# Optimization experiments

Measured on AMD Instinct MI355X. Metric: run time of the kernel, lower is better.

## Reference

```python
import jax, jax.numpy as jnp
import numpy as np

IH, IW = 48, 48           # img_size
C = 256                   # inp == oup
NH, HD = 8, 32            # num_heads, head_dims; inner_dim = 256
HID = 4 * C               # MLP hidden
N = IH * IW               # window size (seq len) = 2304
SCALE = (C // NH) ** -0.5 # (inp_dims // num_heads) ** -0.5
EPS = 1e-5


def _relative_position_index():
    coords = np.stack(np.meshgrid(np.arange(IH), np.arange(IW), indexing='ij'))
    cf = coords.reshape(2, -1)
    rel = (cf[:, :, None] - cf[:, None, :]).transpose(1, 2, 0)
    rel[:, :, 0] += IH - 1
    rel[:, :, 1] += IW - 1
    rel[:, :, 0] *= 2 * IW - 1
    return jnp.asarray(rel.sum(-1).astype(np.int32))  # [N, N]


def setup_inputs() -> dict:
    key = jax.random.key(0)
    ks = jax.random.split(key, 12)
    s = 0.02
    return {
        'x': jax.random.normal(ks[0], (1, IH, IW, C), jnp.float32),
        'gamma1': jnp.ones((C,), jnp.float32),
        'beta1': jnp.zeros((C,), jnp.float32),
        'w_qkv': jax.random.normal(ks[1], (C, 3 * NH * HD), jnp.float32) * s,
        'w_proj': jax.random.normal(ks[2], (NH * HD, C), jnp.float32) * s,
        'b_proj': jnp.zeros((C,), jnp.float32),
        'bias_table': jax.random.normal(ks[3], ((2 * IH - 1) * (2 * IW - 1), NH), jnp.float32) * s,
        'gamma2': jnp.ones((C,), jnp.float32),
        'beta2': jnp.zeros((C,), jnp.float32),
        'w_fc1': jax.random.normal(ks[4], (C, HID), jnp.float32) * s,
        'b_fc1': jnp.zeros((HID,), jnp.float32),
        'w_fc2': jax.random.normal(ks[5], (HID, C), jnp.float32) * s,
        'b_fc2': jnp.zeros((C,), jnp.float32),
        'rel_idx': _relative_position_index(),
    }


def _layernorm(x, g, b):
    mu = jnp.mean(x, axis=-1, keepdims=True)
    var = jnp.mean(jnp.square(x - mu), axis=-1, keepdims=True)
    return (x - mu) * jax.lax.rsqrt(var + EPS) * g + b


def reference(x, gamma1, beta1, w_qkv, w_proj, b_proj, bias_table,
              gamma2, beta2, w_fc1, b_fc1, w_fc2, b_fc2, rel_idx):
    shortcut = x                                   # [1, IH, IW, C]
    t = x.reshape(1, N, C)
    t = _layernorm(t, gamma1, beta1)

    # qkv: [1, N, 3*NH*HD] -> q, k, v each [1, NH, N, HD]
    qkv = (t @ w_qkv).reshape(1, N, 3, NH, HD).transpose(2, 0, 3, 1, 4)
    q, k, v = qkv[0], qkv[1], qkv[2]
    q = q * SCALE

    attn = jnp.einsum('bhnd,bhmd->bhnm', q, k)     # [1, NH, N, N]
    # relative position bias: gather table rows by index -> [NH, N, N]
    bias = bias_table[rel_idx.reshape(-1)].reshape(N, N, NH).transpose(2, 0, 1)
    attn = jax.nn.softmax(attn + bias[None], axis=-1)

    o = jnp.einsum('bhnm,bhmd->bhnd', attn, v)     # [1, NH, N, HD]
    o = o.transpose(0, 2, 1, 3).reshape(1, N, NH * HD)
    o = o @ w_proj + b_proj                        # [1, N, C]

    x = shortcut + o.reshape(1, IH, IW, C)
    shortcut = x

    t = _layernorm(x.reshape(1, N, C), gamma2, beta2)
    t = jax.nn.gelu(t @ w_fc1 + b_fc1, approximate=False) @ w_fc2 + b_fc2
    return shortcut + t.reshape(1, IH, IW, C)
```

## Files before the change

### kernel.cpp

```cpp
#include <hip/hip_runtime.h>
#include <hip/hip_bf16.h>
#include <math.h>

#define IH 48
#define IW 48
#define NN 2304
#define CC 256
#define NH 8
#define HD 32
#define HID 1024
#define NBIAS 9025
#define SCALE 0.17677669529663687f
#define LOG2E 1.4426950408889634f
#define LN_EPS 1e-5f

typedef __attribute__((ext_vector_type(8))) short bf16x8;
typedef __attribute__((ext_vector_type(4))) float f32x4;

__device__ __forceinline__ short f2b(float f) {
    __hip_bfloat16 h = __float2bfloat16(f);
    short s; __builtin_memcpy(&s, &h, 2); return s;
}
__device__ __forceinline__ float b2f(short s) {
    __hip_bfloat16 h; __builtin_memcpy(&h, &s, 2); return __bfloat162float(h);
}
__device__ __forceinline__ float fast_exp2(float x) {
#if __has_builtin(__builtin_amdgcn_exp2f)
    return __builtin_amdgcn_exp2f(x);
#else
    return exp2f(x);
#endif
}

__global__ void prep_kernel(const float* __restrict__ x, const float* __restrict__ g,
                            const float* __restrict__ b, short* __restrict__ t1,
                            const float* __restrict__ bt, short* __restrict__ o_bias)
{
    const int bid = blockIdx.x, tid = threadIdx.x;
    if (bid < NN) {
        __shared__ float red[8];
        float v = x[bid * CC + tid];
        float s = v, s2 = v * v;
        #pragma unroll
        for (int off = 32; off > 0; off >>= 1) {
            s  += __shfl_xor(s, off);
            s2 += __shfl_xor(s2, off);
        }
        const int wid = tid >> 6;
        if ((tid & 63) == 0) { red[wid * 2] = s; red[wid * 2 + 1] = s2; }
        __syncthreads();
        float tot  = red[0] + red[2] + red[4] + red[6];
        float tot2 = red[1] + red[3] + red[5] + red[7];
        float mu   = tot * (1.0f / CC);
        float var  = tot2 * (1.0f / CC) - mu * mu;
        float rstd = rsqrtf(var + LN_EPS);
        t1[bid * CC + tid] = f2b((v - mu) * rstd * g[tid] + b[tid]);
        return;
    }
    const int stride = (gridDim.x - NN) * 256;
    for (int i = (bid - NN) * 256 + tid; i < NBIAS * NH; i += stride) {
        int idx = i >> 3, h = i & 7;
        o_bias[h * NBIAS + idx] = f2b(bt[i] * LOG2E);
    }
}

__global__ void wtrans_kernel(const float* __restrict__ w_qkv, const float* __restrict__ w_proj,
                              const float* __restrict__ w_fc1, const float* __restrict__ w_fc2,
                              short* __restrict__ o_qkv, short* __restrict__ o_proj,
                              short* __restrict__ o_fc1, short* __restrict__ o_fc2)
{
    __shared__ float t[32][33];
    int b = blockIdx.x;
    const float* src; short* dst; int K, Nn, kt, nt;
    if (b < 192)      { src = w_qkv;  dst = o_qkv;  K = 256;  Nn = 768;  kt = b / 24; nt = b % 24; }
    else if (b < 256) { b -= 192; src = w_proj; dst = o_proj; K = 256;  Nn = 256;  kt = b / 8;  nt = b % 8; }
    else if (b < 512) { b -= 256; src = w_fc1;  dst = o_fc1;  K = 256;  Nn = 1024; kt = b / 32; nt = b % 32; }
    else              { b -= 512; src = w_fc2;  dst = o_fc2;  K = 1024; Nn = 256;  kt = b / 8;  nt = b % 8; }
    const int r = threadIdx.x >> 5, c = threadIdx.x & 31;
    const int k0 = kt * 32, n0 = nt * 32;
    #pragma unroll
    for (int i = 0; i < 4; ++i)
        t[r + i * 8][c] = src[(k0 + r + i * 8) * Nn + n0 + c];
    __syncthreads();
    #pragma unroll
    for (int i = 0; i < 4; ++i)
        dst[(n0 + r + i * 8) * K + k0 + c] = f2b(t[c][r + i * 8]);
}

__global__ void ln_kernel(const float* __restrict__ p0, const float* __restrict__ p1,
                          const float* __restrict__ bp, const float* __restrict__ x_in,
                          const float* __restrict__ g, const float* __restrict__ b,
                          short* __restrict__ t2, float* __restrict__ x2)
{
    __shared__ float red[8];
    const int row = blockIdx.x, tid = threadIdx.x;
    const int i = row * CC + tid;
    float v = p0[i] + p1[i] + bp[tid] + x_in[i];
    x2[i] = v;
    float s = v, s2 = v * v;
    #pragma unroll
    for (int off = 32; off > 0; off >>= 1) {
        s  += __shfl_xor(s, off);
        s2 += __shfl_xor(s2, off);
    }
    const int wid = tid >> 6;
    if ((tid & 63) == 0) { red[wid * 2] = s; red[wid * 2 + 1] = s2; }
    __syncthreads();
    float tot  = red[0] + red[2] + red[4] + red[6];
    float tot2 = red[1] + red[3] + red[5] + red[7];
    float mu   = tot * (1.0f / CC);
    float var  = tot2 * (1.0f / CC) - mu * mu;
    float rstd = rsqrtf(var + LN_EPS);
    t2[i] = f2b((v - mu) * rstd * g[tid] + b[tid]);
}

#define GSTRIDE 72
template<int KLEN, int KSTR>
__device__ __forceinline__ void mfma_gemm_core(const short* __restrict__ A,
                                               const short* __restrict__ BT,
                                               int m0, int n0, int kb, f32x4 acc[4],
                                               short* lds)
{
    short* As = lds;
    short* Bs = lds + 64 * GSTRIDE;
    const int tid  = threadIdx.x;
    const int w    = tid >> 6, lane = tid & 63;
    const int quad = lane >> 4, l15 = lane & 15;
    const int sr = tid >> 2;
    const int sc = (tid & 3) * 16;
    #pragma unroll
    for (int c = 0; c < 4; ++c) acc[c] = (f32x4){0.f, 0.f, 0.f, 0.f};

    const short* Ap = &A [(m0 + sr) * KSTR + kb + sc];
    const short* Bp = &BT[(n0 + sr) * KSTR + kb + sc];
    bf16x8 ra0 = *(const bf16x8*)Ap,       ra1 = *(const bf16x8*)(Ap + 8);
    bf16x8 rb0 = *(const bf16x8*)Bp,       rb1 = *(const bf16x8*)(Bp + 8);

    for (int k0 = 0; k0 < KLEN; k0 += 64) {
        __syncthreads();
        *(bf16x8*)&As[sr * GSTRIDE + sc]     = ra0;
        *(bf16x8*)&As[sr * GSTRIDE + sc + 8] = ra1;
        *(bf16x8*)&Bs[sr * GSTRIDE + sc]     = rb0;
        *(bf16x8*)&Bs[sr * GSTRIDE + sc + 8] = rb1;
        if (k0 + 64 < KLEN) {
            ra0 = *(const bf16x8*)(Ap + k0 + 64);
            ra1 = *(const bf16x8*)(Ap + k0 + 72);
            rb0 = *(const bf16x8*)(Bp + k0 + 64);
            rb1 = *(const bf16x8*)(Bp + k0 + 72);
        }
        __syncthreads();
        #pragma unroll
        for (int s = 0; s < 2; ++s) {
            bf16x8 a = *(const bf16x8*)&As[(w * 16 + l15) * GSTRIDE + s * 32 + quad * 8];
            #pragma unroll
            for (int c = 0; c < 4; ++c) {
                bf16x8 b = *(const bf16x8*)&Bs[(c * 16 + l15) * GSTRIDE + s * 32 + quad * 8];
                acc[c] = __builtin_amdgcn_mfma_f32_16x16x32_bf16(a, b, acc[c], 0, 0, 0);
            }
        }
    }
}

__global__ void qkv_kernel(const short* __restrict__ t1, const short* __restrict__ wT,
                           short* __restrict__ qb, short* __restrict__ kb,
                           short* __restrict__ vT)
{
    __shared__ short lds[2 * 64 * GSTRIDE];
    f32x4 acc[4];
    const int m0 = blockIdx.y * 64, n0 = blockIdx.x * 64;
    mfma_gemm_core<256, 256>(t1, wT, m0, n0, 0, acc, lds);
    const int lane = threadIdx.x & 63, w = threadIdx.x >> 6;
    const int quad = lane >> 4, l15 = lane & 15;
    #pragma unroll
    for (int c = 0; c < 4; ++c) {
        int col = n0 + c * 16 + l15;
        int three = col >> 8, rem = col & 255;
        int h = rem >> 5, d = rem & 31;
        #pragma unroll
        for (int r = 0; r < 4; ++r) {
            int row = m0 + w * 16 + quad * 4 + r;
            float v = acc[c][r];
            if (three == 0)      qb[(h * NN + row) * HD + d] = f2b(v * (SCALE * LOG2E));
            else if (three == 1) kb[(h * NN + row) * HD + d] = f2b(v);
            else                 vT[(h * HD + d) * NN + row] = f2b(v);
        }
    }
}

#define PSTRIDE 40
__global__ __launch_bounds__(256) void attn_kernel(
        const short* __restrict__ qb, const short* __restrict__ kb,
        const short* __restrict__ vT, const short* __restrict__ biasT,
        short* __restrict__ o)
{
    __shared__ float Ored[4][16][33];
    __shared__ float lred[4][16];
    __shared__ short sbuf[4][16 * PSTRIDE];
    __shared__ short bwin[48][64];
    const int w = threadIdx.x >> 6, lane = threadIdx.x & 63;
    const int quad = lane >> 4, l15 = lane & 15;
    const int h = blockIdx.x / 144, q0 = (blockIdx.x % 144) * 16;
    const int t0 = w * 576;
    short* sb = &sbuf[w][0];
    const short* bt = &biasT[h * NBIAS];

    const int qi = q0 / IW, qj0 = q0 % IW;

    for (int idx = threadIdx.x; idx < 48 * 63; idx += 256) {
        int kr = idx / 63, cc = idx - kr * 63;
        bwin[kr][cc] = bt[(qi - kr + 47) * 95 + qj0 + cc];
    }

    bf16x8 qf = *(const bf16x8*)&qb[(h * NN + q0 + l15) * HD + quad * 8];

    f32x4 O0 = (f32x4){0.f,0.f,0.f,0.f}, O1 = (f32x4){0.f,0.f,0.f,0.f};
    float lp[4] = {0.f, 0.f, 0.f, 0.f};
    const f32x4 zero = (f32x4){0.f,0.f,0.f,0.f};

    __syncthreads();

    for (int c = 0; c < 18; ++c) {
        const int t = t0 + c * 32;
        bf16x8 k0f = *(const bf16x8*)&kb[(h * NN + t      + l15) * HD + quad * 8];
        bf16x8 k1f = *(const bf16x8*)&kb[(h * NN + t + 16 + l15) * HD + quad * 8];
        f32x4 s0 = __builtin_amdgcn_mfma_f32_16x16x32_bf16(qf, k0f, zero, 0, 0, 0);
        f32x4 s1 = __builtin_amdgcn_mfma_f32_16x16x32_bf16(qf, k1f, zero, 0, 0, 0);
        bf16x8 v0 = *(const bf16x8*)&vT[(h * HD + l15)      * NN + t + quad * 8];
        bf16x8 v1 = *(const bf16x8*)&vT[(h * HD + 16 + l15) * NN + t + quad * 8];

        const int ki0 = t / IW,        kj0_ = t - ki0 * IW;
        const int ki1 = (t + 16) / IW, kj1_ = (t + 16) - ki1 * IW;
        const int cA = quad * 4 + 47 - kj0_ - l15;
        const int cB = quad * 4 + 47 - kj1_ - l15;

        #pragma unroll
        for (int r = 0; r < 4; ++r) {
            float p0 = fast_exp2(s0[r] + b2f(bwin[ki0][cA + r]));
            float p1 = fast_exp2(s1[r] + b2f(bwin[ki1][cB + r]));
            lp[r] += p0 + p1;
            sb[(quad * 4 + r) * PSTRIDE + l15]      = f2b(p0);
            sb[(quad * 4 + r) * PSTRIDE + 16 + l15] = f2b(p1);
        }
        asm volatile("s_waitcnt lgkmcnt(0)" ::: "memory");
        bf16x8 pa = *(const bf16x8*)&sb[l15 * PSTRIDE + quad * 8];
        O0 = __builtin_amdgcn_mfma_f32_16x16x32_bf16(pa, v0, O0, 0, 0, 0);
        O1 = __builtin_amdgcn_mfma_f32_16x16x32_bf16(pa, v1, O1, 0, 0, 0);
    }

    #pragma unroll
    for (int r = 0; r < 4; ++r) {
        float l = lp[r];
        l += __shfl_xor(l, 1); l += __shfl_xor(l, 2);
        l += __shfl_xor(l, 4); l += __shfl_xor(l, 8);
        if (l15 == 0) lred[w][quad * 4 + r] = l;
        Ored[w][quad * 4 + r][l15]      = O0[r];
        Ored[w][quad * 4 + r][16 + l15] = O1[r];
    }
    __syncthreads();
    {
        const int col = threadIdx.x & 31;
        for (int rr = threadIdx.x >> 5; rr < 16; rr += 8) {
            float s = 0.f, l = 0.f;
            #pragma unroll
            for (int pw = 0; pw < 4; ++pw) { s += Ored[pw][rr][col]; l += lred[pw][rr]; }
            o[(q0 + rr) * CC + h * HD + col] = f2b(s / l);
        }
    }
}

__global__ void proj_kernel(const short* __restrict__ o, const short* __restrict__ wT,
                            float* __restrict__ Ppj)
{
    __shared__ short lds[2 * 64 * GSTRIDE];
    f32x4 acc[4];
    const int m0 = blockIdx.y * 64, n0 = blockIdx.x * 64, z = blockIdx.z;
    mfma_gemm_core<128, 256>(o, wT, m0, n0, z * 128, acc, lds);
    const int lane = threadIdx.x & 63, w = threadIdx.x >> 6;
    const int quad = lane >> 4, l15 = lane & 15;
    float* out = Ppj + z * (NN * CC);
    #pragma unroll
    for (int c = 0; c < 4; ++c) {
        int col = n0 + c * 16 + l15;
        #pragma unroll
        for (int r = 0; r < 4; ++r) {
            int row = m0 + w * 16 + quad * 4 + r;
            out[row * CC + col] = acc[c][r];
        }
    }
}

__global__ void fc1_kernel(const short* __restrict__ t2, const short* __restrict__ wT,
                           const float* __restrict__ bias, short* __restrict__ h1)
{
    __shared__ short lds[2 * 64 * GSTRIDE];
    f32x4 acc[4];
    const int m0 = blockIdx.y * 64, n0 = blockIdx.x * 64;
    mfma_gemm_core<256, 256>(t2, wT, m0, n0, 0, acc, lds);
    const int lane = threadIdx.x & 63, w = threadIdx.x >> 6;
    const int quad = lane >> 4, l15 = lane & 15;
    #pragma unroll
    for (int c = 0; c < 4; ++c) {
        int col = n0 + c * 16 + l15;
        #pragma unroll
        for (int r = 0; r < 4; ++r) {
            int row = m0 + w * 16 + quad * 4 + r;
            float v = acc[c][r] + bias[col];
            float ge = 0.5f * v * (1.0f + erff(v * 0.7071067811865476f));
            h1[row * HID + col] = f2b(ge);
        }
    }
}

__global__ void fc2_kernel(const short* __restrict__ h1, const short* __restrict__ wT,
                           float* __restrict__ Pfc)
{
    __shared__ short lds[2 * 64 * GSTRIDE];
    f32x4 acc[4];
    const int m0 = blockIdx.y * 64, n0 = blockIdx.x * 64, z = blockIdx.z;
    mfma_gemm_core<512, 1024>(h1, wT, m0, n0, z * 512, acc, lds);
    const int lane = threadIdx.x & 63, w = threadIdx.x >> 6;
    const int quad = lane >> 4, l15 = lane & 15;
    float* out = Pfc + z * (NN * CC);
    #pragma unroll
    for (int c = 0; c < 4; ++c) {
        int col = n0 + c * 16 + l15;
        #pragma unroll
        for (int r = 0; r < 4; ++r) {
            int row = m0 + w * 16 + quad * 4 + r;
            out[row * CC + col] = acc[c][r];
        }
    }
}

__global__ void fc2_red(const float* __restrict__ Pfc, const float* __restrict__ bias,
                        const float* __restrict__ x2, float* __restrict__ out)
{
    const int i = blockIdx.x * CC + threadIdx.x;
    const int NC = NN * CC;
    out[i] = Pfc[i] + Pfc[NC + i] + bias[threadIdx.x] + x2[i];
}

extern "C" void kernel_launch(void* const* d_in, const int* in_sizes, int n_in,
                              void* d_out, int out_size, void* d_ws, size_t ws_size,
                              hipStream_t stream)
{
    const float* x          = (const float*)d_in[0];
    const float* gamma1     = (const float*)d_in[1];
    const float* beta1      = (const float*)d_in[2];
    const float* w_qkv      = (const float*)d_in[3];
    const float* w_proj     = (const float*)d_in[4];
    const float* b_proj     = (const float*)d_in[5];
    const float* bias_table = (const float*)d_in[6];
    const float* gamma2     = (const float*)d_in[7];
    const float* beta2      = (const float*)d_in[8];
    const float* w_fc1      = (const float*)d_in[9];
    const float* b_fc1      = (const float*)d_in[10];
    const float* w_fc2      = (const float*)d_in[11];
    const float* b_fc2      = (const float*)d_in[12];

    short* S = (short*)d_ws;
    const int NC = NN * CC;
    short* t1     = S;
    short* qb     = t1  + NC;
    short* kb     = qb  + NC;
    short* vT     = kb  + NC;
    short* obuf   = vT  + NC;
    short* t2     = obuf+ NC;
    short* h1     = t2  + NC;
    short* wTqkv  = h1  + NN * HID;
    short* wTproj = wTqkv  + 768 * 256;
    short* wTfc1  = wTproj + 256 * 256;
    short* wTfc2  = wTfc1  + 1024 * 256;
    short* biasT  = wTfc2  + 256 * 1024;
    float* x2     = (float*)(biasT + NH * NBIAS + 8);
    float* Ppj    = (float*)t1;
    float* Pfc    = (float*)t1;

    prep_kernel<<<NN + 64, 256, 0, stream>>>(x, gamma1, beta1, t1,
                                             bias_table, biasT);
    wtrans_kernel<<<768, 256, 0, stream>>>(w_qkv, w_proj, w_fc1, w_fc2,
                                           wTqkv, wTproj, wTfc1, wTfc2);
    qkv_kernel<<<dim3(12, 36), 256, 0, stream>>>(t1, wTqkv, qb, kb, vT);
    attn_kernel<<<1152, 256, 0, stream>>>(qb, kb, vT, biasT, obuf);
    proj_kernel<<<dim3(4, 36, 2), 256, 0, stream>>>(obuf, wTproj, Ppj);
    ln_kernel<<<NN, 256, 0, stream>>>(Ppj, Ppj + NC, b_proj, x,
                                      gamma2, beta2, t2, x2);
    fc1_kernel<<<dim3(16, 36), 256, 0, stream>>>(t2, wTfc1, b_fc1, h1);
    fc2_kernel<<<dim3(4, 36, 2), 256, 0, stream>>>(h1, wTfc2, Pfc);
    fc2_red<<<NN, 256, 0, stream>>>(Pfc, b_fc2, x2, (float*)d_out);
}
```

Measured before the change: 169.1 us.

## Drop split-K partials in proj/fc2, fuse bias+residual epilogues, merge weight transpose into prep

Merges the weight-transpose kernel into the prep kernel, saving one launch. The proj and fc2 GEMMs stop using a two-way split-K with fp32 partial buffers. They now run full K with 32-row tiles and 128-thread blocks, adding bias and residual in the epilogue. This removes the separate fc2 reduction kernel and the partial-sum traffic, and ln_kernel now only normalizes x2. The cost is longer per-block K loops with fewer waves per block, which reduces latency hiding in the GEMMs.

```diff
diff --git a/kernel.cpp b/kernel.cpp
--- a/kernel.cpp
+++ b/kernel.cpp
@@ -34,11 +34,16 @@
 
 __global__ void prep_kernel(const float* __restrict__ x, const float* __restrict__ g,
                             const float* __restrict__ b, short* __restrict__ t1,
-                            const float* __restrict__ bt, short* __restrict__ o_bias)
-{
+                            const float* __restrict__ bt, short* __restrict__ o_bias,
+                            const float* __restrict__ w_qkv, const float* __restrict__ w_proj,
+                            const float* __restrict__ w_fc1, const float* __restrict__ w_fc2,
+                            short* __restrict__ o_qkv, short* __restrict__ o_proj,
+                            short* __restrict__ o_fc1, short* __restrict__ o_fc2)
+{
+    __shared__ float tsh[32][33];
+    __shared__ float red[8];
     const int bid = blockIdx.x, tid = threadIdx.x;
     if (bid < NN) {
-        __shared__ float red[8];
         float v = x[bid * CC + tid];
         float s = v, s2 = v * v;
         #pragma unroll
@@ -57,46 +62,39 @@
         t1[bid * CC + tid] = f2b((v - mu) * rstd * g[tid] + b[tid]);
         return;
     }
-    const int stride = (gridDim.x - NN) * 256;
-    for (int i = (bid - NN) * 256 + tid; i < NBIAS * NH; i += stride) {
+    if (bid < NN + 768) {
+        int bb = bid - NN;
+        const float* src; short* dst; int K, Nn, kt, nt;
+        if (bb < 192)      { src = w_qkv;  dst = o_qkv;  K = 256;  Nn = 768;  kt = bb / 24; nt = bb % 24; }
+        else if (bb < 256) { bb -= 192; src = w_proj; dst = o_proj; K = 256;  Nn = 256;  kt = bb / 8;  nt = bb % 8; }
+        else if (bb < 512) { bb -= 256; src = w_fc1;  dst = o_fc1;  K = 256;  Nn = 1024; kt = bb / 32; nt = bb % 32; }
+        else               { bb -= 512; src = w_fc2;  dst = o_fc2;  K = 1024; Nn = 256;  kt = bb / 8;  nt = bb % 8; }
+        const int r = tid >> 5, c = tid & 31;
+        const int k0 = kt * 32, n0 = nt * 32;
+        #pragma unroll
+        for (int i = 0; i < 4; ++i)
+            tsh[r + i * 8][c] = src[(k0 + r + i * 8) * Nn + n0 + c];
+        __syncthreads();
+        #pragma unroll
+        for (int i = 0; i < 4; ++i)
+            dst[(n0 + r + i * 8) * K + k0 + c] = f2b(tsh[c][r + i * 8]);
+        return;
+    }
+    const int stride = (gridDim.x - NN - 768) * 256;
+    for (int i = (bid - NN - 768) * 256 + tid; i < NBIAS * NH; i += stride) {
         int idx = i >> 3, h = i & 7;
         o_bias[h * NBIAS + idx] = f2b(bt[i] * LOG2E);
     }
 }
 
-__global__ void wtrans_kernel(const float* __restrict__ w_qkv, const float* __restrict__ w_proj,
-                              const float* __restrict__ w_fc1, const float* __restrict__ w_fc2,
-                              short* __restrict__ o_qkv, short* __restrict__ o_proj,
-                              short* __restrict__ o_fc1, short* __restrict__ o_fc2)
-{
-    __shared__ float t[32][33];
-    int b = blockIdx.x;
-    const float* src; short* dst; int K, Nn, kt, nt;
-    if (b < 192)      { src = w_qkv;  dst = o_qkv;  K = 256;  Nn = 768;  kt = b / 24; nt = b % 24; }
-    else if (b < 256) { b -= 192; src = w_proj; dst = o_proj; K = 256;  Nn = 256;  kt = b / 8;  nt = b % 8; }
-    else if (b < 512) { b -= 256; src = w_fc1;  dst = o_fc1;  K = 256;  Nn = 1024; kt = b / 32; nt = b % 32; }
-    else              { b -= 512; src = w_fc2;  dst = o_fc2;  K = 1024; Nn = 256;  kt = b / 8;  nt = b % 8; }
-    const int r = threadIdx.x >> 5, c = threadIdx.x & 31;
-    const int k0 = kt * 32, n0 = nt * 32;
-    #pragma unroll
-    for (int i = 0; i < 4; ++i)
-        t[r + i * 8][c] = src[(k0 + r + i * 8) * Nn + n0 + c];
-    __syncthreads();
-    #pragma unroll
-    for (int i = 0; i < 4; ++i)
-        dst[(n0 + r + i * 8) * K + k0 + c] = f2b(t[c][r + i * 8]);
-}
-
-__global__ void ln_kernel(const float* __restrict__ p0, const float* __restrict__ p1,
-                          const float* __restrict__ bp, const float* __restrict__ x_in,
-                          const float* __restrict__ g, const float* __restrict__ b,
-                          short* __restrict__ t2, float* __restrict__ x2)
+__global__ void ln_kernel(const float* __restrict__ x,
+                          const float* __restrict__ g,
+                          const float* __restrict__ b,
+                          short* __restrict__ out)
 {
     __shared__ float red[8];
     const int row = blockIdx.x, tid = threadIdx.x;
-    const int i = row * CC + tid;
-    float v = p0[i] + p1[i] + bp[tid] + x_in[i];
-    x2[i] = v;
+    float v = x[row * CC + tid];
     float s = v, s2 = v * v;
     #pragma unroll
     for (int off = 32; off > 0; off >>= 1) {
@@ -111,18 +109,18 @@
     float mu   = tot * (1.0f / CC);
     float var  = tot2 * (1.0f / CC) - mu * mu;
     float rstd = rsqrtf(var + LN_EPS);
-    t2[i] = f2b((v - mu) * rstd * g[tid] + b[tid]);
+    out[row * CC + tid] = f2b((v - mu) * rstd * g[tid] + b[tid]);
 }
 
 #define GSTRIDE 72
-template<int KLEN, int KSTR>
+template<int KLEN, int KSTR, int TM>
 __device__ __forceinline__ void mfma_gemm_core(const short* __restrict__ A,
                                                const short* __restrict__ BT,
                                                int m0, int n0, int kb, f32x4 acc[4],
                                                short* lds)
 {
     short* As = lds;
-    short* Bs = lds + 64 * GSTRIDE;
+    short* Bs = lds + TM * GSTRIDE;
     const int tid  = threadIdx.x;
     const int w    = tid >> 6, lane = tid & 63;
     const int quad = lane >> 4, l15 = lane & 15;
@@ -135,6 +133,12 @@
     const short* Bp = &BT[(n0 + sr) * KSTR + kb + sc];
     bf16x8 ra0 = *(const bf16x8*)Ap,       ra1 = *(const bf16x8*)(Ap + 8);
     bf16x8 rb0 = *(const bf16x8*)Bp,       rb1 = *(const bf16x8*)(Bp + 8);
+    bf16x8 rc0, rc1;
+    const short* Bp2 = Bp;
+    if constexpr (TM == 32) {
+        Bp2 = &BT[(n0 + sr + 32) * KSTR + kb + sc];
+        rc0 = *(const bf16x8*)Bp2;  rc1 = *(const bf16x8*)(Bp2 + 8);
+    }
 
     for (int k0 = 0; k0 < KLEN; k0 += 64) {
         __syncthreads();
@@ -142,11 +146,19 @@
         *(bf16x8*)&As[sr * GSTRIDE + sc + 8] = ra1;
         *(bf16x8*)&Bs[sr * GSTRIDE + sc]     = rb0;
         *(bf16x8*)&Bs[sr * GSTRIDE + sc + 8] = rb1;
+        if constexpr (TM == 32) {
+            *(bf16x8*)&Bs[(sr + 32) * GSTRIDE + sc]     = rc0;
+            *(bf16x8*)&Bs[(sr + 32) * GSTRIDE + sc + 8] = rc1;
+        }
         if (k0 + 64 < KLEN) {
             ra0 = *(const bf16x8*)(Ap + k0 + 64);
             ra1 = *(const bf16x8*)(Ap + k0 + 72);
             rb0 = *(const bf16x8*)(Bp + k0 + 64);
             rb1 = *(const bf16x8*)(Bp + k0 + 72);
+            if constexpr (TM == 32) {
+                rc0 = *(const bf16x8*)(Bp2 + k0 + 64);
+                rc1 = *(const bf16x8*)(Bp2 + k0 + 72);
+            }
         }
         __syncthreads();
         #pragma unroll
@@ -168,7 +180,7 @@
     __shared__ short lds[2 * 64 * GSTRIDE];
     f32x4 acc[4];
     const int m0 = blockIdx.y * 64, n0 = blockIdx.x * 64;
-    mfma_gemm_core<256, 256>(t1, wT, m0, n0, 0, acc, lds);
+    mfma_gemm_core<256, 256, 64>(t1, wT, m0, n0, 0, acc, lds);
     const int lane = threadIdx.x & 63, w = threadIdx.x >> 6;
     const int quad = lane >> 4, l15 = lane & 15;
     #pragma unroll
@@ -269,22 +281,22 @@
 }
 
 __global__ void proj_kernel(const short* __restrict__ o, const short* __restrict__ wT,
-                            float* __restrict__ Ppj)
-{
-    __shared__ short lds[2 * 64 * GSTRIDE];
+                            const float* __restrict__ bias, const float* __restrict__ x_in,
+                            float* __restrict__ x2)
+{
+    __shared__ short lds[(32 + 64) * GSTRIDE];
     f32x4 acc[4];
-    const int m0 = blockIdx.y * 64, n0 = blockIdx.x * 64, z = blockIdx.z;
-    mfma_gemm_core<128, 256>(o, wT, m0, n0, z * 128, acc, lds);
+    const int m0 = blockIdx.y * 32, n0 = blockIdx.x * 64;
+    mfma_gemm_core<256, 256, 32>(o, wT, m0, n0, 0, acc, lds);
     const int lane = threadIdx.x & 63, w = threadIdx.x >> 6;
     const int quad = lane >> 4, l15 = lane & 15;
-    float* out = Ppj + z * (NN * CC);
     #pragma unroll
     for (int c = 0; c < 4; ++c) {
         int col = n0 + c * 16 + l15;
         #pragma unroll
         for (int r = 0; r < 4; ++r) {
             int row = m0 + w * 16 + quad * 4 + r;
-            out[row * CC + col] = acc[c][r];
+            x2[row * CC + col] = acc[c][r] + bias[col] + x_in[row * CC + col];
         }
     }
 }
@@ -295,7 +307,7 @@
     __shared__ short lds[2 * 64 * GSTRIDE];
     f32x4 acc[4];
     const int m0 = blockIdx.y * 64, n0 = blockIdx.x * 64;
-    mfma_gemm_core<256, 256>(t2, wT, m0, n0, 0, acc, lds);
+    mfma_gemm_core<256, 256, 64>(t2, wT, m0, n0, 0, acc, lds);
     const int lane = threadIdx.x & 63, w = threadIdx.x >> 6;
     const int quad = lane >> 4, l15 = lane & 15;
     #pragma unroll
@@ -312,32 +324,24 @@
 }
 
 __global__ void fc2_kernel(const short* __restrict__ h1, const short* __restrict__ wT,
-                           float* __restrict__ Pfc)
-{
-    __shared__ short lds[2 * 64 * GSTRIDE];
+                           const float* __restrict__ bias, const float* __restrict__ x2,
+                           float* __restrict__ out)
+{
+    __shared__ short lds[(32 + 64) * GSTRIDE];
     f32x4 acc[4];
-    const int m0 = blockIdx.y * 64, n0 = blockIdx.x * 64, z = blockIdx.z;
-    mfma_gemm_core<512, 1024>(h1, wT, m0, n0, z * 512, acc, lds);
+    const int m0 = blockIdx.y * 32, n0 = blockIdx.x * 64;
+    mfma_gemm_core<1024, 1024, 32>(h1, wT, m0, n0, 0, acc, lds);
     const int lane = threadIdx.x & 63, w = threadIdx.x >> 6;
     const int quad = lane >> 4, l15 = lane & 15;
-    float* out = Pfc + z * (NN * CC);
     #pragma unroll
     for (int c = 0; c < 4; ++c) {
         int col = n0 + c * 16 + l15;
         #pragma unroll
         for (int r = 0; r < 4; ++r) {
             int row = m0 + w * 16 + quad * 4 + r;
-            out[row * CC + col] = acc[c][r];
-        }
-    }
-}
-
-__global__ void fc2_red(const float* __restrict__ Pfc, const float* __restrict__ bias,
-                        const float* __restrict__ x2, float* __restrict__ out)
-{
-    const int i = blockIdx.x * CC + threadIdx.x;
-    const int NC = NN * CC;
-    out[i] = Pfc[i] + Pfc[NC + i] + bias[threadIdx.x] + x2[i];
+            out[row * CC + col] = acc[c][r] + bias[col] + x2[row * CC + col];
+        }
+    }
 }
 
 extern "C" void kernel_launch(void* const* d_in, const int* in_sizes, int n_in,
@@ -373,19 +377,16 @@
     short* wTfc2  = wTfc1  + 1024 * 256;
     short* biasT  = wTfc2  + 256 * 1024;
     float* x2     = (float*)(biasT + NH * NBIAS + 8);
-    float* Ppj    = (float*)t1;
-    float* Pfc    = (float*)t1;
-
-    prep_kernel<<<NN + 64, 256, 0, stream>>>(x, gamma1, beta1, t1,
-                                             bias_table, biasT);
-    wtrans_kernel<<<768, 256, 0, stream>>>(w_qkv, w_proj, w_fc1, w_fc2,
-                                           wTqkv, wTproj, wTfc1, wTfc2);
+
+    prep_kernel<<<NN + 768 + 64, 256, 0, stream>>>(x, gamma1, beta1, t1,
+                                                   bias_table, biasT,
+                                                   w_qkv, w_proj, w_fc1, w_fc2,
+                                                   wTqkv, wTproj, wTfc1, wTfc2);
     qkv_kernel<<<dim3(12, 36), 256, 0, stream>>>(t1, wTqkv, qb, kb, vT);
     attn_kernel<<<1152, 256, 0, stream>>>(qb, kb, vT, biasT, obuf);
-    proj_kernel<<<dim3(4, 36, 2), 256, 0, stream>>>(obuf, wTproj, Ppj);
-    ln_kernel<<<NN, 256, 0, stream>>>(Ppj, Ppj + NC, b_proj, x,
-                                      gamma2, beta2, t2, x2);
+    proj_kernel<<<dim3(4, 72), 128, 0, stream>>>(obuf, wTproj, b_proj, x, x2);
+    ln_kernel<<<NN, 256, 0, stream>>>(x2, gamma2, beta2, t2);
     fc1_kernel<<<dim3(16, 36), 256, 0, stream>>>(t2, wTfc1, b_fc1, h1);
-    fc2_kernel<<<dim3(4, 36, 2), 256, 0, stream>>>(h1, wTfc2, Pfc);
-    fc2_red<<<NN, 256, 0, stream>>>(Pfc, b_fc2, x2, (float*)d_out);
-}
+    fc2_kernel<<<dim3(4, 72), 128, 0, stream>>>(h1, wTfc2, b_fc2, x2,
+                                                (float*)d_out);
+}
```

Result: faster. 161.0 us (-4.8%).
